# Performance work log

Measured on AMD Instinct MI355X. Metric: run time of the kernel, lower is better.

The kernel has to match this reference:

```python
import jax, jax.numpy as jnp
import numpy as np

B, C_IN, C_OUT, H, W = 4, 256, 256, 64, 64


def conv1x1(x, w, b):
    # x: [B, Cin, H, W], w: [Cout, Cin], b: [Cout]
    return jnp.einsum('bchw,oc->bohw', x, w) + b[None, :, None, None]


def setup_inputs() -> dict:
    key = jax.random.key(0)
    ks = jax.random.split(key, 12)
    s_in = 1.0 / np.sqrt(C_IN)
    s_out = 1.0 / np.sqrt(C_OUT)
    return {
        'query_input': jax.random.normal(ks[0], (B, C_IN, H, W), jnp.float32),
        'key_value_input': jax.random.normal(ks[1], (B, C_IN, H, W), jnp.float32),
        'Wq': jax.random.uniform(ks[2], (C_OUT, C_IN), jnp.float32, -s_in, s_in),
        'bq': jax.random.uniform(ks[3], (C_OUT,), jnp.float32, -s_in, s_in),
        'Wk': jax.random.uniform(ks[4], (C_OUT, C_IN), jnp.float32, -s_in, s_in),
        'bk': jax.random.uniform(ks[5], (C_OUT,), jnp.float32, -s_in, s_in),
        'Wv': jax.random.uniform(ks[6], (C_OUT, C_IN), jnp.float32, -s_in, s_in),
        'bv': jax.random.uniform(ks[7], (C_OUT,), jnp.float32, -s_in, s_in),
        'W1': jax.random.uniform(ks[8], (C_OUT, C_OUT), jnp.float32, -s_out, s_out),
        'b1': jax.random.uniform(ks[9], (C_OUT,), jnp.float32, -s_out, s_out),
        'W2': jax.random.uniform(ks[10], (C_OUT, C_OUT), jnp.float32, -s_out, s_out),
        'b2': jax.random.uniform(ks[11], (C_OUT,), jnp.float32, -s_out, s_out),
    }


def reference(query_input, key_value_input, Wq, bq, Wk, bk, Wv, bv, W1, b1, W2, b2):
    q = conv1x1(query_input, Wq, bq)            # [B, Co, H, W]
    k = conv1x1(key_value_input, Wk, bk)
    v = conv1x1(key_value_input, Wv, bv)
    b, co, h, w = q.shape
    n = h * w
    qf = q.reshape(b, co, n)                    # [B, Co, N]
    kf = k.reshape(b, co, n)
    vf = v.reshape(b, co, n)
    # scores: q^T k over channels -> [B, N, N], softmax over keys (last dim)
    attn = jax.nn.softmax(jnp.einsum('bcn,bcm->bnm', qf, kf), axis=-1)
    # attended value: [B, Co, N] -> [B, Co, H, W]
    av = jnp.einsum('bnm,bcm->bcn', attn, vf).reshape(b, co, h, w)
    hid = jax.nn.relu(conv1x1(av, W1, b1))
    return conv1x1(hid, W2, b2)
```

## Files before the change

kernel.cpp:

```cpp
#include <hip/hip_runtime.h>
#include <math.h>

#define CCH 256
#define NPIX 4096
#define NB 4
#define NTOT (NB * NPIX)

typedef _Float16 f16;
typedef f16 f16x8 __attribute__((ext_vector_type(8)));
typedef __fp16 fp16x2 __attribute__((ext_vector_type(2)));
typedef float f32x4 __attribute__((ext_vector_type(4)));
typedef unsigned short u16;
typedef unsigned int u32;

__device__ __forceinline__ u16 f2h(float f) {
  union { f16 h; u16 u; } c; c.h = (f16)f; return c.u;
}
__device__ __forceinline__ void fsplit(float v, u16& h, u16& l) {
  union { f16 h; u16 u; } a, b;
  a.h = (f16)v;
  b.h = (f16)(v - (float)a.h);
  h = a.u; l = b.u;
}
__device__ __forceinline__ u32 pkh(float a, float b) {
  union { fp16x2 v; u32 u; } c;
  c.v = __builtin_amdgcn_cvt_pkrtz(a, b);
  return c.u;
}
__device__ __forceinline__ u32 shflu(u32 v, int s) { return (u32)__shfl((int)v, s, 64); }
__device__ __forceinline__ f32x4 mm(f16x8 a, f16x8 b, f32x4 c) {
  return __builtin_amdgcn_mfma_f32_16x16x32_f16(a, b, c, 0, 0, 0);
}
__device__ __forceinline__ f16x8 ld8(const u16* p) {
  return *reinterpret_cast<const f16x8*>(p);
}

using gas_t = const __attribute__((address_space(1))) void*;
using las_t = __attribute__((address_space(3))) void*;
__device__ __forceinline__ void gl2lds16(const void* g, void* l) {
  __builtin_amdgcn_global_load_lds((gas_t)g, (las_t)l, 16, 0, 0);
}

__global__ __launch_bounds__(256) void prep_w(
    const float* w0, const float* w1, const float* w2, const float* w3,
    const float* w4, u16* wp)
{
  const float* srcs[5] = {w0, w1, w2, w3, w4};
  const int m = blockIdx.y;
  const float* s = srcs[m];
  u16* ph = wp + (size_t)m * 2 * 65536;
  u16* pl = ph + 65536;
  const int i = (blockIdx.x * 256 + threadIdx.x) * 4;
  float4 v = *reinterpret_cast<const float4*>(s + i);
  ushort4 hv, lv;
  fsplit(v.x, hv.x, lv.x); fsplit(v.y, hv.y, lv.y);
  fsplit(v.z, hv.z, lv.z); fsplit(v.w, hv.w, lv.w);
  *reinterpret_cast<ushort4*>(ph + i) = hv;
  *reinterpret_cast<ushort4*>(pl + i) = lv;
}

__global__ __launch_bounds__(256) void transpose_split(
    const float* xq, const float* xkv,
    u16* xqTh, u16* xqTl, u16* xkvTh, u16* xkvTl)
{
  __shared__ float T[64][65];
  const int nb = blockIdx.x * 64, cb = blockIdx.y * 64;
  const int z = blockIdx.z, b = z & 3, inp = z >> 2;
  const float* src = (inp ? xkv : xq) + (size_t)b * CCH * NPIX;
  u16* dh = inp ? xkvTh : xqTh;
  u16* dl = inp ? xkvTl : xqTl;
  const int t = threadIdx.x;
  #pragma unroll
  for (int k = 0; k < 4; ++k) {
    int e = t + 256 * k;
    int c = e >> 4, n4 = e & 15;
    float4 v = *reinterpret_cast<const float4*>(&src[(size_t)(cb + c) * NPIX + nb + n4 * 4]);
    T[c][n4 * 4 + 0] = v.x; T[c][n4 * 4 + 1] = v.y;
    T[c][n4 * 4 + 2] = v.z; T[c][n4 * 4 + 3] = v.w;
  }
  __syncthreads();
  const int n = t >> 2, cq = t & 3, c0 = cq * 16;
  alignas(16) u16 hh[16], ll[16];
  #pragma unroll
  for (int j = 0; j < 16; ++j) fsplit(T[c0 + j][n], hh[j], ll[j]);
  size_t base = ((size_t)b * NPIX + nb + n) * CCH + cb + c0;
  *reinterpret_cast<uint4*>(&dh[base])     = *reinterpret_cast<uint4*>(hh);
  *reinterpret_cast<uint4*>(&dh[base + 8]) = *reinterpret_cast<uint4*>(hh + 8);
  *reinterpret_cast<uint4*>(&dl[base])     = *reinterpret_cast<uint4*>(ll);
  *reinterpret_cast<uint4*>(&dl[base + 8]) = *reinterpret_cast<uint4*>(ll + 8);
}

template<int PL, int OM>
__global__ __launch_bounds__(512) void conv_s0(
    const u16* __restrict__ Ah, const u16* __restrict__ Al,
    const u16* __restrict__ Wh, const u16* __restrict__ Wl,
    const float* __restrict__ bias, u16* __restrict__ Oh, u16* __restrict__ Ol)
{
  __shared__ alignas(16) u16 sA[PL * 64 * 256];
  const int nb = blockIdx.x * 64, ob = blockIdx.y * 128;
  const int tid = threadIdx.x, wid = tid >> 6, lane = tid & 63;
  const int gg = lane >> 4, x = lane & 15;
  const int wn = wid & 1, wo = wid >> 1;

  f16x8 bh[2][8], bl[2][8];
  #pragma unroll
  for (int os = 0; os < 2; ++os) {
    const int row = ob + wo * 32 + os * 16 + x;
    #pragma unroll
    for (int kc = 0; kc < 8; ++kc) {
      bh[os][kc] = ld8(&Wh[(size_t)row * 256 + kc * 32 + gg * 8]);
      bl[os][kc] = ld8(&Wl[(size_t)row * 256 + kc * 32 + gg * 8]);
    }
  }
  const u16* Ap[2] = {Ah, Al};
  #pragma unroll
  for (int p = 0; p < PL; ++p)
    #pragma unroll
    for (int r = 0; r < 4; ++r) {
      int e = tid + 512 * r;
      int row = e >> 5, ch = e & 31;
      gl2lds16(Ap[p] + (size_t)(nb + row) * 256 + ((ch ^ (row & 7)) * 8),
               &sA[p * 16384 + e * 8]);
    }
  __syncthreads();

  f32x4 acc[2][2] = {};
  #pragma unroll
  for (int ms = 0; ms < 2; ++ms) {
    const int row = wn * 32 + ms * 16 + x;
    #pragma unroll
    for (int kc = 0; kc < 8; ++kc) {
      const int off = row * 256 + ((kc * 4 + gg) ^ (x & 7)) * 8;
      f16x8 a0 = ld8(&sA[off]);
      #pragma unroll
      for (int os = 0; os < 2; ++os) {
        acc[ms][os] = mm(a0, bh[os][kc], acc[ms][os]);
        acc[ms][os] = mm(a0, bl[os][kc], acc[ms][os]);
      }
      if (PL == 2) {
        f16x8 a1 = ld8(&sA[16384 + off]);
        #pragma unroll
        for (int os = 0; os < 2; ++os)
          acc[ms][os] = mm(a1, bh[os][kc], acc[ms][os]);
      }
    }
  }
  #pragma unroll
  for (int os = 0; os < 2; ++os) {
    const float bo = bias[ob + wo * 32 + os * 16 + x];
    const size_t col = ob + wo * 32 + os * 16 + x;
    #pragma unroll
    for (int ms = 0; ms < 2; ++ms)
      #pragma unroll
      for (int j = 0; j < 4; ++j) {
        float val = acc[ms][os][j] + bo;
        size_t row = nb + wn * 32 + ms * 16 + gg * 4 + j;
        if (OM == 1) {
          Oh[row * 256 + col] = f2h(fmaxf(val, 0.f));
        } else {
          u16 h, l; fsplit(val, h, l);
          Oh[row * 256 + col] = h;
          Ol[row * 256 + col] = l;
        }
      }
  }
}

template<int PL, int OM>
__global__ __launch_bounds__(512) void conv_s1(
    const u16* __restrict__ Wh, const u16* __restrict__ Wl,
    const u16* __restrict__ Bh, const u16* __restrict__ Bl,
    const float* __restrict__ bias, void* __restrict__ Out)
{
  __shared__ alignas(16) u16 sB[PL * 64 * 256];
  const int nb = blockIdx.x * 64, ob = blockIdx.y * 128;
  const int tid = threadIdx.x, wid = tid >> 6, lane = tid & 63;
  const int gg = lane >> 4, x = lane & 15;
  const int wn = wid & 1, wo = wid >> 1;

  f16x8 ah[2][8], al[2][8];
  #pragma unroll
  for (int as = 0; as < 2; ++as) {
    const int row = ob + wo * 32 + as * 16 + x;
    #pragma unroll
    for (int kc = 0; kc < 8; ++kc) {
      ah[as][kc] = ld8(&Wh[(size_t)row * 256 + kc * 32 + gg * 8]);
      al[as][kc] = ld8(&Wl[(size_t)row * 256 + kc * 32 + gg * 8]);
    }
  }
  const u16* Bp[2] = {Bh, Bl};
  #pragma unroll
  for (int p = 0; p < PL; ++p)
    #pragma unroll
    for (int r = 0; r < 4; ++r) {
      int e = tid + 512 * r;
      int row = e >> 5, ch = e & 31;
      gl2lds16(Bp[p] + (size_t)(nb + row) * 256 + ((ch ^ (row & 7)) * 8),
               &sB[p * 16384 + e * 8]);
    }
  __syncthreads();

  f32x4 acc[2][2] = {};
  #pragma unroll
  for (int ns = 0; ns < 2; ++ns) {
    const int row = wn * 32 + ns * 16 + x;
    #pragma unroll
    for (int kc = 0; kc < 8; ++kc) {
      const int off = row * 256 + ((kc * 4 + gg) ^ (x & 7)) * 8;
      f16x8 b0 = ld8(&sB[off]);
      #pragma unroll
      for (int as = 0; as < 2; ++as) {
        acc[as][ns] = mm(ah[as][kc], b0, acc[as][ns]);
        acc[as][ns] = mm(al[as][kc], b0, acc[as][ns]);
      }
      if (PL == 2) {
        f16x8 b1 = ld8(&sB[16384 + off]);
        #pragma unroll
        for (int as = 0; as < 2; ++as)
          acc[as][ns] = mm(ah[as][kc], b1, acc[as][ns]);
      }
    }
  }
  #pragma unroll
  for (int as = 0; as < 2; ++as)
    #pragma unroll
    for (int j = 0; j < 4; ++j) {
      const int o = ob + wo * 32 + as * 16 + gg * 4 + j;
      const float bo = bias[o];
      #pragma unroll
      for (int ns = 0; ns < 2; ++ns) {
        int nf = nb + wn * 32 + ns * 16 + x;
        float val = acc[as][ns][j] + bo;
        int b_ = nf >> 12, n_ = nf & 4095;
        size_t addr = ((size_t)b_ * 256 + o) * 4096 + n_;
        if (OM == 1) ((float*)Out)[addr] = val;
        else         ((u16*)Out)[addr] = f2h(val);
      }
    }
}

__global__ __launch_bounds__(512) void attn_mfma(
    const u16* __restrict__ Qh, const u16* __restrict__ Ql,
    const u16* __restrict__ Kh, const u16* __restrict__ Kl,
    const u16* __restrict__ Vs, u16* __restrict__ AVt)
{
  __shared__ alignas(16) u16 smem[49152];
  __shared__ float sMm[2][64], sMl[2][64];
  u16* sKh = smem;
  u16* sKl = smem + 16384;
  u16* sV  = smem + 32768;

  const int b = blockIdx.y, qb = blockIdx.x * 64;
  const int tid = threadIdx.x, wid = tid >> 6;
  const int g = wid & 3, par = wid >> 2;
  const int lane = tid & 63, gg = lane >> 4, x = lane & 15;

  f16x8 qh[8], ql[8];
  {
    const u16* qhp = Qh + ((size_t)b * NPIX + qb + g * 16 + x) * CCH;
    const u16* qlp = Ql + ((size_t)b * NPIX + qb + g * 16 + x) * CCH;
    #pragma unroll
    for (int kc = 0; kc < 8; ++kc) {
      qh[kc] = ld8(qhp + kc * 32 + gg * 8);
      ql[kc] = ld8(qlp + kc * 32 + gg * 8);
    }
  }
  int kSrc[4], kDst[4], vSrc[4], vDst[4];
  #pragma unroll
  for (int r = 0; r < 4; ++r) {
    int e = tid + 512 * r;
    int m = e >> 5, ch = e & 31;
    kSrc[r] = m * CCH + ((ch ^ (m & 7)) * 8);
    kDst[r] = e * 8;
    int c = e >> 3, c2 = e & 7;
    vSrc[r] = c * NPIX + ((c2 ^ (c & 7)) * 8);
    vDst[r] = e * 8;
  }
  const u16* KhB = Kh + (size_t)b * NPIX * CCH;
  const u16* KlB = Kl + (size_t)b * NPIX * CCH;
  const u16* VB  = Vs + (size_t)b * CCH * NPIX;

  f32x4 Oacc[16];
  #pragma unroll
  for (int i = 0; i < 16; ++i) Oacc[i] = f32x4{0.f, 0.f, 0.f, 0.f};
  float m_run = -INFINITY, l_run = 0.f;

  #pragma unroll
  for (int r = 0; r < 4; ++r) {
    gl2lds16(KhB + kSrc[r], &sKh[kDst[r]]);
    gl2lds16(KlB + kSrc[r], &sKl[kDst[r]]);
    gl2lds16(VB + vSrc[r], &sV[vDst[r]]);
  }
  __syncthreads();

  for (int mt = 0; mt < 64; ++mt) {
    f32x4 St[2];
    St[0] = f32x4{0.f, 0.f, 0.f, 0.f};
    St[1] = f32x4{0.f, 0.f, 0.f, 0.f};
    #pragma unroll
    for (int msub = 0; msub < 2; ++msub) {
      const int rb = (par * 32 + msub * 16 + x) * CCH;
      #pragma unroll
      for (int kc = 0; kc < 8; ++kc) {
        const int off = rb + ((kc * 4 + gg) ^ (x & 7)) * 8;
        f16x8 ah_ = ld8(&sKh[off]);
        f16x8 al_ = ld8(&sKl[off]);
        St[msub] = mm(ah_, qh[kc], St[msub]);
        St[msub] = mm(ah_, ql[kc], St[msub]);
        St[msub] = mm(al_, qh[kc], St[msub]);
      }
    }
    __syncthreads();

    if (mt + 1 < 64) {
      const size_t ko = (size_t)(mt + 1) * 64 * CCH;
      #pragma unroll
      for (int r = 0; r < 4; ++r) {
        gl2lds16(KhB + ko + kSrc[r], &sKh[kDst[r]]);
        gl2lds16(KlB + ko + kSrc[r], &sKl[kDst[r]]);
      }
    }

    float vmax = fmaxf(fmaxf(fmaxf(St[0][0], St[0][1]), fmaxf(St[0][2], St[0][3])),
                       fmaxf(fmaxf(St[1][0], St[1][1]), fmaxf(St[1][2], St[1][3])));
    vmax = fmaxf(vmax, __shfl_xor(vmax, 16, 64));
    vmax = fmaxf(vmax, __shfl_xor(vmax, 32, 64));
    float alpha = 1.f;
    if (!__all(vmax <= m_run + 8.f)) {
      const float mnew = fmaxf(m_run, vmax);
      alpha = __expf(m_run - mnew);
      m_run = mnew;
      #pragma unroll
      for (int i = 0; i < 16; ++i) Oacc[i] *= alpha;
    }
    float p[2][4], ps = 0.f;
    #pragma unroll
    for (int msx = 0; msx < 2; ++msx)
      #pragma unroll
      for (int r = 0; r < 4; ++r) {
        p[msx][r] = __expf(St[msx][r] - m_run);
        ps += p[msx][r];
      }
    ps += __shfl_xor(ps, 16, 64);
    ps += __shfl_xor(ps, 32, 64);
    l_run = l_run * alpha + ps;

    u32 Pp[2][2];
    #pragma unroll
    for (int msx = 0; msx < 2; ++msx) {
      Pp[msx][0] = pkh(p[msx][0], p[msx][1]);
      Pp[msx][1] = pkh(p[msx][2], p[msx][3]);
    }
    const int src0 = ((gg & 1) * 2) * 16 + x, src1 = src0 + 16;
    const bool sel = (gg >> 1) != 0;
    union { u32 u[4]; f16x8 v; } pb;
    {
      u32 a0 = shflu(Pp[0][0], src0), a1 = shflu(Pp[1][0], src0);
      u32 b0 = shflu(Pp[0][1], src0), b1 = shflu(Pp[1][1], src0);
      u32 c0 = shflu(Pp[0][0], src1), c1 = shflu(Pp[1][0], src1);
      u32 d0 = shflu(Pp[0][1], src1), d1 = shflu(Pp[1][1], src1);
      pb.u[0] = sel ? a1 : a0;
      pb.u[1] = sel ? b1 : b0;
      pb.u[2] = sel ? c1 : c0;
      pb.u[3] = sel ? d1 : d0;
    }

    #pragma unroll
    for (int cs = 0; cs < 16; ++cs) {
      const int off = (cs * 16 + x) * 64 + ((par * 4 + gg) ^ (x & 7)) * 8;
      Oacc[cs] = mm(ld8(&sV[off]), pb.v, Oacc[cs]);
    }
    __syncthreads();

    if (mt + 1 < 64) {
      const size_t vo = (size_t)(mt + 1) * 64;
      #pragma unroll
      for (int r = 0; r < 4; ++r)
        gl2lds16(VB + vo + vSrc[r], &sV[vDst[r]]);
    }
  }

  const int q = g * 16 + x;
  if (gg == 0) { sMm[par][q] = m_run; sMl[par][q] = l_run; }
  __syncthreads();
  const float mo = sMm[1 - par][q], lo = sMl[1 - par][q];
  const float mtot = fmaxf(m_run, mo);
  const float w = __expf(m_run - mtot), wo_ = __expf(mo - mtot);
  const float lt = l_run * w + lo * wo_;
  const float sc = w / lt;
  #pragma unroll
  for (int i = 0; i < 16; ++i) Oacc[i] *= sc;

  float* Obuf = reinterpret_cast<float*>(smem);
  #define OFF_(G, C, X) ((G) * 4360 + (C) * 17 + (X))
  if (par == 1) {
    #pragma unroll
    for (int cs = 0; cs < 16; ++cs)
      #pragma unroll
      for (int r = 0; r < 4; ++r)
        Obuf[OFF_(g, cs * 16 + gg * 4 + r, x)] = Oacc[cs][r];
  }
  __syncthreads();
  if (par == 0) {
    #pragma unroll
    for (int cs = 0; cs < 16; ++cs)
      #pragma unroll
      for (int r = 0; r < 4; ++r)
        Obuf[OFF_(g, cs * 16 + gg * 4 + r, x)] += Oacc[cs][r];
  }
  __syncthreads();
  const int n_loc = tid & 63, cq = tid >> 6;
  const int g2 = n_loc >> 4, x2 = n_loc & 15, c0 = cq * 32;
  alignas(16) u32 wds[16];
  #pragma unroll
  for (int j = 0; j < 16; ++j)
    wds[j] = pkh(Obuf[OFF_(g2, c0 + 2 * j, x2)], Obuf[OFF_(g2, c0 + 2 * j + 1, x2)]);
  u16* dst = AVt + ((size_t)b * NPIX + qb + n_loc) * CCH + c0;
  #pragma unroll
  for (int k = 0; k < 4; ++k)
    *reinterpret_cast<uint4*>(dst + k * 8) = *reinterpret_cast<uint4*>(&wds[k * 4]);
}

extern "C" void kernel_launch(void* const* d_in, const int* in_sizes, int n_in,
                              void* d_out, int out_size, void* d_ws, size_t ws_size,
                              hipStream_t stream) {
  const float* x_q  = (const float*)d_in[0];
  const float* x_kv = (const float*)d_in[1];
  const float* Wq = (const float*)d_in[2];
  const float* bq = (const float*)d_in[3];
  const float* Wk = (const float*)d_in[4];
  const float* bk = (const float*)d_in[5];
  const float* Wv = (const float*)d_in[6];
  const float* bv = (const float*)d_in[7];
  const float* W1 = (const float*)d_in[8];
  const float* b1 = (const float*)d_in[9];
  const float* W2 = (const float*)d_in[10];
  const float* b2 = (const float*)d_in[11];
  float* out = (float*)d_out;

  u16* ws = (u16*)d_ws;
  const size_t P = (size_t)NTOT * CCH;
  u16* xqTh  = ws;
  u16* xqTl  = ws + P;
  u16* xkvTh = ws + 2 * P;
  u16* xkvTl = ws + 3 * P;
  u16* Wp    = ws + 4 * P;
  u16* Whq = Wp + 0 * 65536, *Wlq = Wp + 1 * 65536;
  u16* Whk = Wp + 2 * 65536, *Wlk = Wp + 3 * 65536;
  u16* Whv = Wp + 4 * 65536, *Wlv = Wp + 5 * 65536;
  u16* Wh1 = Wp + 6 * 65536, *Wl1 = Wp + 7 * 65536;
  u16* Wh2 = Wp + 8 * 65536, *Wl2 = Wp + 9 * 65536;
  u16* base2 = Wp + 10 * 65536;
  u16* Qhp = base2 + 0 * P;
  u16* Qlp = base2 + 1 * P;
  u16* Khp = base2 + 2 * P;
  u16* Klp = base2 + 3 * P;
  u16* Vhp = base2 + 4 * P;
  u16* AVt  = xqTh;
  u16* HIDt = xqTl;

  prep_w<<<dim3(64, 5), 256, 0, stream>>>(Wq, Wk, Wv, W1, W2, Wp);
  transpose_split<<<dim3(64, 4, 8), 256, 0, stream>>>(
      x_q, x_kv, xqTh, xqTl, xkvTh, xkvTl);

  conv_s0<2, 0><<<dim3(256, 2), 512, 0, stream>>>(xqTh, xqTl, Whq, Wlq, bq, Qhp, Qlp);
  conv_s0<2, 0><<<dim3(256, 2), 512, 0, stream>>>(xkvTh, xkvTl, Whk, Wlk, bk, Khp, Klp);
  conv_s1<2, 0><<<dim3(256, 2), 512, 0, stream>>>(Whv, Wlv, xkvTh, xkvTl, bv, (void*)Vhp);

  attn_mfma<<<dim3(NPIX / 64, NB), 512, 0, stream>>>(Qhp, Qlp, Khp, Klp, Vhp, AVt);

  conv_s0<1, 1><<<dim3(256, 2), 512, 0, stream>>>(AVt, nullptr, Wh1, Wl1, b1, HIDt, nullptr);
  conv_s1<1, 1><<<dim3(256, 2), 512, 0, stream>>>(Wh2, Wl2, HIDt, nullptr, b2, (void*)out);
}
```

Measured before the change: 398.1 us.

## Fuse K/V projections, new LDS swizzle, stage V in double-width tiles

Merges the separate K and V 1x1 conv launches into one kernel, so the shared key/value input tile is loaded into LDS once and half the waves compute K while the other half compute V. Replaces the XOR-by-row-low-bits LDS swizzle with a wider swizzle in all conv and attention kernels, aimed at cutting bank conflicts on the 16-byte MFMA operand reads. The attention kernel's V buffer grows to 128 keys per stage, reloaded every other iteration, which lowers sync and issue overhead for V loads. This raises LDS use to 128 KB per block, which may cut occupancy.

Result: faster. 389.6 us (-2.1%).

```diff
diff --git a/kernel.cpp b/kernel.cpp
--- a/kernel.cpp
+++ b/kernel.cpp
@@ -33,6 +33,19 @@
 }
 __device__ __forceinline__ f16x8 ld8(const u16* p) {
   return *reinterpret_cast<const f16x8*>(p);
+}
+
+__device__ __forceinline__ int swz_rd(int c, int x) {
+  return c ^ x ^ ((c & 3) << 3);
+}
+__device__ __forceinline__ int swz_st(int s, int r) {
+  return s ^ (r & 15) ^ (((s ^ r) & 3) << 3);
+}
+__device__ __forceinline__ int swzv_rd(int c, int x) {
+  return c ^ x ^ ((c & 3) << 2);
+}
+__device__ __forceinline__ int swzv_st(int s, int r) {
+  return s ^ (r & 15) ^ (((s ^ r) & 3) << 2);
 }
 
 using gas_t = const __attribute__((address_space(1))) void*;
@@ -118,9 +131,9 @@
     #pragma unroll
     for (int r = 0; r < 4; ++r) {
       int e = tid + 512 * r;
-      int row = e >> 5, ch = e & 31;
-      gl2lds16(Ap[p] + (size_t)(nb + row) * 256 + ((ch ^ (row & 7)) * 8),
-               &sA[p * 16384 + e * 8]);
+      int row = e >> 5, s = e & 31;
+      int c = swz_st(s, row);
+      gl2lds16(Ap[p] + (size_t)(nb + row) * 256 + c * 8, &sA[p * 16384 + e * 8]);
     }
   __syncthreads();
 
@@ -130,7 +143,7 @@
     const int row = wn * 32 + ms * 16 + x;
     #pragma unroll
     for (int kc = 0; kc < 8; ++kc) {
-      const int off = row * 256 + ((kc * 4 + gg) ^ (x & 7)) * 8;
+      const int off = row * 256 + swz_rd(kc * 4 + gg, x) * 8;
       f16x8 a0 = ld8(&sA[off]);
       #pragma unroll
       for (int os = 0; os < 2; ++os) {
@@ -194,9 +207,9 @@
     #pragma unroll
     for (int r = 0; r < 4; ++r) {
       int e = tid + 512 * r;
-      int row = e >> 5, ch = e & 31;
-      gl2lds16(Bp[p] + (size_t)(nb + row) * 256 + ((ch ^ (row & 7)) * 8),
-               &sB[p * 16384 + e * 8]);
+      int row = e >> 5, s = e & 31;
+      int c = swz_st(s, row);
+      gl2lds16(Bp[p] + (size_t)(nb + row) * 256 + c * 8, &sB[p * 16384 + e * 8]);
     }
   __syncthreads();
 
@@ -206,7 +219,7 @@
     const int row = wn * 32 + ns * 16 + x;
     #pragma unroll
     for (int kc = 0; kc < 8; ++kc) {
-      const int off = row * 256 + ((kc * 4 + gg) ^ (x & 7)) * 8;
+      const int off = row * 256 + swz_rd(kc * 4 + gg, x) * 8;
       f16x8 b0 = ld8(&sB[off]);
       #pragma unroll
       for (int as = 0; as < 2; ++as) {
@@ -239,12 +252,111 @@
     }
 }
 
+__global__ __launch_bounds__(512) void conv_kv(
+    const u16* __restrict__ xh, const u16* __restrict__ xl,
+    const u16* __restrict__ Wkh, const u16* __restrict__ Wkl,
+    const u16* __restrict__ Wvh, const u16* __restrict__ Wvl,
+    const float* __restrict__ bk, const float* __restrict__ bv,
+    u16* __restrict__ Kh, u16* __restrict__ Kl, u16* __restrict__ Vh)
+{
+  __shared__ alignas(16) u16 sA[2 * 64 * 256];
+  const int nb = blockIdx.x * 64, ob = blockIdx.y * 128;
+  const int tid = threadIdx.x, wid = tid >> 6, lane = tid & 63;
+  const int gg = lane >> 4, x = lane & 15;
+  const int part = wid >> 2;
+  const int wo = wid & 3;
+
+  const u16* Wh = part ? Wvh : Wkh;
+  const u16* Wl = part ? Wvl : Wkl;
+  f16x8 wh[2][8], wl[2][8];
+  #pragma unroll
+  for (int os = 0; os < 2; ++os) {
+    const int row = ob + wo * 32 + os * 16 + x;
+    #pragma unroll
+    for (int kc = 0; kc < 8; ++kc) {
+      wh[os][kc] = ld8(&Wh[(size_t)row * 256 + kc * 32 + gg * 8]);
+      wl[os][kc] = ld8(&Wl[(size_t)row * 256 + kc * 32 + gg * 8]);
+    }
+  }
+  const u16* Ap[2] = {xh, xl};
+  #pragma unroll
+  for (int p = 0; p < 2; ++p)
+    #pragma unroll
+    for (int r = 0; r < 4; ++r) {
+      int e = tid + 512 * r;
+      int row = e >> 5, s = e & 31;
+      int c = swz_st(s, row);
+      gl2lds16(Ap[p] + (size_t)(nb + row) * 256 + c * 8, &sA[p * 16384 + e * 8]);
+    }
+  __syncthreads();
+
+  f32x4 acc[4][2] = {};
+  #pragma unroll
+  for (int ns = 0; ns < 4; ++ns) {
+    const int row = ns * 16 + x;
+    #pragma unroll
+    for (int kc = 0; kc < 8; ++kc) {
+      const int off = row * 256 + swz_rd(kc * 4 + gg, x) * 8;
+      f16x8 a0 = ld8(&sA[off]);
+      f16x8 a1 = ld8(&sA[16384 + off]);
+      if (part == 0) {
+        #pragma unroll
+        for (int os = 0; os < 2; ++os) {
+          acc[ns][os] = mm(a0, wh[os][kc], acc[ns][os]);
+          acc[ns][os] = mm(a0, wl[os][kc], acc[ns][os]);
+          acc[ns][os] = mm(a1, wh[os][kc], acc[ns][os]);
+        }
+      } else {
+        #pragma unroll
+        for (int os = 0; os < 2; ++os) {
+          acc[ns][os] = mm(wh[os][kc], a0, acc[ns][os]);
+          acc[ns][os] = mm(wl[os][kc], a0, acc[ns][os]);
+          acc[ns][os] = mm(wh[os][kc], a1, acc[ns][os]);
+        }
+      }
+    }
+  }
+
+  if (part == 0) {
+    #pragma unroll
+    for (int os = 0; os < 2; ++os) {
+      const int o = ob + wo * 32 + os * 16 + x;
+      const float bo = bk[o];
+      #pragma unroll
+      for (int ns = 0; ns < 4; ++ns)
+        #pragma unroll
+        for (int j = 0; j < 4; ++j) {
+          float val = acc[ns][os][j] + bo;
+          u16 h, l; fsplit(val, h, l);
+          size_t row = nb + ns * 16 + gg * 4 + j;
+          Kh[row * 256 + o] = h;
+          Kl[row * 256 + o] = l;
+        }
+    }
+  } else {
+    #pragma unroll
+    for (int os = 0; os < 2; ++os)
+      #pragma unroll
+      for (int j = 0; j < 4; ++j) {
+        const int o = ob + wo * 32 + os * 16 + gg * 4 + j;
+        const float bo = bv[o];
+        #pragma unroll
+        for (int ns = 0; ns < 4; ++ns) {
+          int nf = nb + ns * 16 + x;
+          float val = acc[ns][os][j] + bo;
+          int b_ = nf >> 12, n_ = nf & 4095;
+          Vh[((size_t)b_ * 256 + o) * 4096 + n_] = f2h(val);
+        }
+      }
+  }
+}
+
 __global__ __launch_bounds__(512) void attn_mfma(
     const u16* __restrict__ Qh, const u16* __restrict__ Ql,
     const u16* __restrict__ Kh, const u16* __restrict__ Kl,
     const u16* __restrict__ Vs, u16* __restrict__ AVt)
 {
-  __shared__ alignas(16) u16 smem[49152];
+  __shared__ alignas(16) u16 smem[65536];
   __shared__ float sMm[2][64], sMl[2][64];
   u16* sKh = smem;
   u16* sKl = smem + 16384;
@@ -265,32 +377,37 @@
       ql[kc] = ld8(qlp + kc * 32 + gg * 8);
     }
   }
-  int kSrc[4], kDst[4], vSrc[4], vDst[4];
-  #pragma unroll
-  for (int r = 0; r < 4; ++r) {
-    int e = tid + 512 * r;
-    int m = e >> 5, ch = e & 31;
-    kSrc[r] = m * CCH + ((ch ^ (m & 7)) * 8);
-    kDst[r] = e * 8;
-    int c = e >> 3, c2 = e & 7;
-    vSrc[r] = c * NPIX + ((c2 ^ (c & 7)) * 8);
-    vDst[r] = e * 8;
-  }
   const u16* KhB = Kh + (size_t)b * NPIX * CCH;
   const u16* KlB = Kl + (size_t)b * NPIX * CCH;
   const u16* VB  = Vs + (size_t)b * CCH * NPIX;
 
+#define STAGE_K(KO) do {                                        \
+    _Pragma("unroll")                                           \
+    for (int j_ = 0; j_ < 4; ++j_) {                            \
+      int e_ = tid + 512 * j_;                                  \
+      int r_ = e_ >> 5, s_ = e_ & 31;                           \
+      int c_ = swz_st(s_, r_);                                  \
+      size_t src_ = (KO) + (size_t)r_ * CCH + c_ * 8;           \
+      gl2lds16(KhB + src_, &sKh[e_ * 8]);                       \
+      gl2lds16(KlB + src_, &sKl[e_ * 8]);                       \
+    } } while (0)
+
+#define STAGE_V(KB) do {                                        \
+    _Pragma("unroll")                                           \
+    for (int j_ = 0; j_ < 8; ++j_) {                            \
+      int e_ = tid + 512 * j_;                                  \
+      int r_ = e_ >> 4, s_ = e_ & 15;                           \
+      int c_ = swzv_st(s_, r_);                                 \
+      gl2lds16(VB + (KB) + (size_t)r_ * NPIX + c_ * 8, &sV[e_ * 8]); \
+    } } while (0)
+
   f32x4 Oacc[16];
   #pragma unroll
   for (int i = 0; i < 16; ++i) Oacc[i] = f32x4{0.f, 0.f, 0.f, 0.f};
   float m_run = -INFINITY, l_run = 0.f;
 
-  #pragma unroll
-  for (int r = 0; r < 4; ++r) {
-    gl2lds16(KhB + kSrc[r], &sKh[kDst[r]]);
-    gl2lds16(KlB + kSrc[r], &sKl[kDst[r]]);
-    gl2lds16(VB + vSrc[r], &sV[vDst[r]]);
-  }
+  STAGE_K((size_t)0);
+  STAGE_V((size_t)0);
   __syncthreads();
 
   for (int mt = 0; mt < 64; ++mt) {
@@ -302,7 +419,7 @@
       const int rb = (par * 32 + msub * 16 + x) * CCH;
       #pragma unroll
       for (int kc = 0; kc < 8; ++kc) {
-        const int off = rb + ((kc * 4 + gg) ^ (x & 7)) * 8;
+        const int off = rb + swz_rd(kc * 4 + gg, x) * 8;
         f16x8 ah_ = ld8(&sKh[off]);
         f16x8 al_ = ld8(&sKl[off]);
         St[msub] = mm(ah_, qh[kc], St[msub]);
@@ -312,14 +429,7 @@
     }
     __syncthreads();
 
-    if (mt + 1 < 64) {
-      const size_t ko = (size_t)(mt + 1) * 64 * CCH;
-      #pragma unroll
-      for (int r = 0; r < 4; ++r) {
-        gl2lds16(KhB + ko + kSrc[r], &sKh[kDst[r]]);
-        gl2lds16(KlB + ko + kSrc[r], &sKl[kDst[r]]);
-      }
-    }
+    if (mt + 1 < 64) STAGE_K((size_t)(mt + 1) * 64 * CCH);
 
     float vmax = fmaxf(fmaxf(fmaxf(St[0][0], St[0][1]), fmaxf(St[0][2], St[0][3])),
                        fmaxf(fmaxf(St[1][0], St[1][1]), fmaxf(St[1][2], St[1][3])));
@@ -365,19 +475,16 @@
       pb.u[3] = sel ? d1 : d0;
     }
 
+    const int ct = ((mt & 1) << 3) + par * 4 + gg;
+    const int sv = swzv_rd(ct, x);
     #pragma unroll
     for (int cs = 0; cs < 16; ++cs) {
-      const int off = (cs * 16 + x) * 64 + ((par * 4 + gg) ^ (x & 7)) * 8;
+      const int off = (cs * 16 + x) * 128 + sv * 8;
       Oacc[cs] = mm(ld8(&sV[off]), pb.v, Oacc[cs]);
     }
     __syncthreads();
 
-    if (mt + 1 < 64) {
-      const size_t vo = (size_t)(mt + 1) * 64;
-      #pragma unroll
-      for (int r = 0; r < 4; ++r)
-        gl2lds16(VB + vo + vSrc[r], &sV[vDst[r]]);
-    }
+    if ((mt & 1) && mt + 1 < 64) STAGE_V((size_t)(mt + 1) * 64);
   }
 
   const int q = g * 16 + x;
@@ -464,8 +571,8 @@
       x_q, x_kv, xqTh, xqTl, xkvTh, xkvTl);
 
   conv_s0<2, 0><<<dim3(256, 2), 512, 0, stream>>>(xqTh, xqTl, Whq, Wlq, bq, Qhp, Qlp);
-  conv_s0<2, 0><<<dim3(256, 2), 512, 0, stream>>>(xkvTh, xkvTl, Whk, Wlk, bk, Khp, Klp);
-  conv_s1<2, 0><<<dim3(256, 2), 512, 0, stream>>>(Whv, Wlv, xkvTh, xkvTl, bv, (void*)Vhp);
+  conv_kv<<<dim3(256, 2), 512, 0, stream>>>(
+      xkvTh, xkvTl, Whk, Wlk, Whv, Wlv, bk, bv, Khp, Klp, Vhp);
 
   attn_mfma<<<dim3(NPIX / 64, NB), 512, 0, stream>>>(Qhp, Qlp, Khp, Klp, Vhp, AVt);
 
```
